# Optimization experiments

Hardware: AMD Instinct MI355X
Metric: run time of the kernel (lower is better)

The kernel has to match this reference:

```python
import jax, jax.numpy as jnp
import numpy as np

N = 20000        # num nodes
E = 320000       # num edges (avg degree 16)
INPUT_DIM = 256
D = 512          # d_model
FF = 2048        # dim_feedforward
OUT = 128        # output_linear out features
HDIM = 8         # LiteMLA per-head dim
KS = 5           # LiteMLA scale kernel size (scales=(5,))


def _layernorm(x, g, b, eps=1e-5):
    m = x.mean(-1, keepdims=True)
    v = ((x - m) ** 2).mean(-1, keepdims=True)
    return (x - m) * jax.lax.rsqrt(v + eps) * g + b


def _pos_encoding():
    # sin/cos table, d_model even branch of PositionalEncoding
    pos = np.arange(N, dtype=np.float32)[:, None]
    div = np.exp(np.arange(0, D, 2, dtype=np.float32) * (-np.log(10000.0) / D))
    pe = np.zeros((N, D), np.float32)
    pe[:, 0::2] = np.sin(pos * div)
    pe[:, 1::2] = np.cos(pos * div)
    return jnp.asarray(pe)


def _lite_mla(h, W_qkv, conv_w, W_proj, b_proj):
    # ReLU linear attention with one extra conv scale (kernel 5), per EfficientViT LiteMLA
    n, d = h.shape
    qkv = h @ W_qkv                               # [N, 3D]
    xc = qkv.T[None]                              # [1, 3D, N]
    ms = jax.lax.conv_general_dilated(
        xc, conv_w, window_strides=(1,), padding='SAME',
        feature_group_count=3 * D)                # depthwise conv over node axis
    ms = ms[0].T                                  # [N, 3D]
    full = jnp.concatenate([qkv, ms], axis=1)     # [N, 6D]
    heads = full.shape[1] // (3 * HDIM)           # 2 * D / HDIM
    t = full.reshape(n, heads, 3, HDIM)
    q = jax.nn.relu(t[:, :, 0])
    k = jax.nn.relu(t[:, :, 1])
    v = t[:, :, 2]
    v1 = jnp.concatenate([v, jnp.ones_like(v[..., :1])], axis=-1)  # append denom row
    kv = jnp.einsum('nhd,nhe->hde', k, v1)        # [h, HDIM, HDIM+1]
    o = jnp.einsum('nhd,hde->nhe', q, kv)         # [N, h, HDIM+1]
    o = o[..., :HDIM] / (o[..., HDIM:] + 1e-15)
    o = o.reshape(n, heads * HDIM)                # [N, 2D]
    return o @ W_proj + b_proj


def _fwd(x, edge_attr, pe, W_in, b_in, W_qkv, conv_w, W_proj, b_proj,
         g1, beta1, W1, bf1, W2, bf2, g2, beta2, W_out, b_out,
         edge_index, num_nodes):
    n = num_nodes
    h = x @ W_in + b_in
    h = h + pe[:n]                                # positional encoding (dropout=eval)
    # add self loops with weight 1
    loop = jnp.arange(n)
    row = jnp.concatenate([edge_index[0], loop])
    col = jnp.concatenate([edge_index[1], loop])
    w = jnp.concatenate([edge_attr, jnp.ones((n,), edge_attr.dtype)])
    # symmetric normalization: D^-1/2 W D^-1/2
    deg = jax.ops.segment_sum(w, row, num_segments=n)
    dis = jnp.where(deg > 0, jax.lax.rsqrt(jnp.maximum(deg, 1e-12)), 0.0)
    nw = dis[row] * w * dis[col]
    # attention + FFN (post-norm residuals as written)
    src2 = _lite_mla(h, W_qkv, conv_w, W_proj, b_proj)
    src = h + _layernorm(src2, g1, beta1)
    ff = jax.nn.relu(src @ W1 + bf1) @ W2 + bf2
    src = src + _layernorm(ff, g2, beta2)
    # sparse adjacency matmul: out[i] = sum_{e: row=i} nw_e * src[col_e]
    agg = jax.ops.segment_sum(nw[:, None] * src[col], row, num_segments=n)
    return jax.nn.relu(agg) @ W_out + b_out      # [N, OUT]


def setup_inputs() -> dict:
    key = jax.random.key(0)
    ks = jax.random.split(key, 10)
    s = lambda i, *sh: jax.random.normal(ks[i], sh, jnp.float32) * 0.02
    f32 = jnp.float32
    return {
        'x': jax.random.normal(ks[0], (N, INPUT_DIM), f32),
        'edge_index': jax.random.randint(ks[1], (2, E), 0, N),
        'edge_attr': jax.random.uniform(ks[2], (E,), f32),
        'num_nodes': N,
        'pe': _pos_encoding(),
        'W_in': s(3, INPUT_DIM, D), 'b_in': jnp.zeros((D,), f32),
        'W_qkv': s(4, D, 3 * D),
        'conv_w': s(5, 3 * D, 1, KS),
        'W_proj': s(6, 2 * D, D), 'b_proj': jnp.zeros((D,), f32),
        'g1': jnp.ones((D,), f32), 'beta1': jnp.zeros((D,), f32),
        'W1': s(7, D, FF), 'bf1': jnp.zeros((FF,), f32),
        'W2': s(8, FF, D), 'bf2': jnp.zeros((D,), f32),
        'g2': jnp.ones((D,), f32), 'beta2': jnp.zeros((D,), f32),
        'W_out': s(9, D, OUT), 'b_out': jnp.zeros((OUT,), f32),
    }


def reference(x, edge_index, edge_attr, num_nodes, pe, W_in, b_in, W_qkv, conv_w,
              W_proj, b_proj, g1, beta1, W1, bf1, W2, bf2, g2, beta2, W_out, b_out):
    return _fwd(x, edge_attr, pe, W_in, b_in, W_qkv, conv_w, W_proj, b_proj,
                g1, beta1, W1, bf1, W2, bf2, g2, beta2, W_out, b_out,
                edge_index, num_nodes)
```

## Files before the change

kernel.cpp:

```cpp
#include <hip/hip_runtime.h>

#define N_NODES 20000
#define N_EDGES 320000
#define DIN     256
#define DMODEL  512
#define TD      1536
#define FFD     2048
#define DOUT    128

typedef _Float16 f16;
typedef f16 f16x8 __attribute__((ext_vector_type(8)));
typedef f16 f16x4 __attribute__((ext_vector_type(4)));
typedef f16 f16x2 __attribute__((ext_vector_type(2)));
typedef float f32x4 __attribute__((ext_vector_type(4)));

__device__ __forceinline__ void cstore(float* p, float v) { *p = v; }
__device__ __forceinline__ void cstore(f16* p, float v)   { *p = (f16)v; }

#if defined(__has_builtin)
#if __has_builtin(__builtin_amdgcn_global_load_lds)
#define USE_GLOAD_LDS 1
#endif
#endif

template<typename TC, int HAS_BIAS, int HAS_ADD, int DO_RELU>
__global__ __launch_bounds__(256)
void gemm_mfma(const f16* __restrict__ A, const f16* __restrict__ Bt,
               const float* __restrict__ bias, const float* __restrict__ addmat,
               TC* __restrict__ C, int M, int N, int K)
{
    __shared__ f16 smem[32768];
    const int tid  = threadIdx.x;
    const int lane = tid & 63;
    const int wid  = tid >> 6;
    const int wm = wid >> 1, wn = wid & 1;

    const int nwg  = gridDim.x;
    const int bid  = blockIdx.x;
    const int q    = nwg >> 3, rres = nwg & 7;
    const int xcd  = bid & 7,  slot = bid >> 3;
    const int wgid = (xcd < rres ? xcd * (q + 1)
                                 : rres * (q + 1) + (xcd - rres) * q) + slot;
    const int ntn  = N >> 7;
    const int m0 = (wgid / ntn) * 128, n0 = (wgid % ntn) * 128;

    f32x4 acc[4][4];
    #pragma unroll
    for (int i = 0; i < 4; ++i)
        #pragma unroll
        for (int j = 0; j < 4; ++j)
            acc[i][j] = (f32x4)0.0f;

    const int r  = lane & 15;
    const int kg = lane >> 4;
    const int px = (kg ^ ((r >> 1) & 3)) << 3;

#ifdef USE_GLOAD_LDS
    const int seg0 = wid * 2, seg1 = wid * 2 + 1;
    const int row0 = seg0 * 16 + (lane >> 2);
    const int row1 = seg1 * 16 + (lane >> 2);
    const int kc0  = (lane & 3) ^ ((row0 >> 1) & 3);
    const int kc1  = (lane & 3) ^ ((row1 >> 1) & 3);
    const f16* a0 = A  + (size_t)(m0 + row0) * K + kc0 * 8;
    const f16* a1 = A  + (size_t)(m0 + row1) * K + kc1 * 8;
    const f16* b0 = Bt + (size_t)(n0 + row0) * K + kc0 * 8;
    const f16* b1 = Bt + (size_t)(n0 + row1) * K + kc1 * 8;

    auto stage = [&](int buf, int k0) {
        f16* as = smem + buf * 4096;
        f16* bs = smem + 16384 + buf * 4096;
        __builtin_amdgcn_global_load_lds(
            (const __attribute__((address_space(1))) void*)(a0 + k0),
            (__attribute__((address_space(3))) void*)&as[seg0 * 512], 16, 0, 0);
        __builtin_amdgcn_global_load_lds(
            (const __attribute__((address_space(1))) void*)(a1 + k0),
            (__attribute__((address_space(3))) void*)&as[seg1 * 512], 16, 0, 0);
        __builtin_amdgcn_global_load_lds(
            (const __attribute__((address_space(1))) void*)(b0 + k0),
            (__attribute__((address_space(3))) void*)&bs[seg0 * 512], 16, 0, 0);
        __builtin_amdgcn_global_load_lds(
            (const __attribute__((address_space(1))) void*)(b1 + k0),
            (__attribute__((address_space(3))) void*)&bs[seg1 * 512], 16, 0, 0);
    };

    const int NT = K >> 5;
    stage(0, 0);
    if (NT > 1) stage(1, 32);
    for (int kt = 0; kt < NT; ++kt) {
        const int cur = kt & 3;
        if (kt + 2 < NT) {
            stage((kt + 2) & 3, (kt + 2) << 5);
            asm volatile("s_waitcnt vmcnt(8)" ::: "memory");
        } else if (kt + 1 < NT) {
            asm volatile("s_waitcnt vmcnt(4)" ::: "memory");
        } else {
            asm volatile("s_waitcnt vmcnt(0)" ::: "memory");
        }
        __builtin_amdgcn_s_barrier();
        __builtin_amdgcn_sched_barrier(0);
        const f16* as = smem + cur * 4096;
        const f16* bs = smem + 16384 + cur * 4096;
        f16x8 af[4], bfr[4];
        #pragma unroll
        for (int m = 0; m < 4; ++m)
            af[m] = *(const f16x8*)(&as[(wm * 64 + m * 16 + r) * 32 + px]);
        #pragma unroll
        for (int n = 0; n < 4; ++n)
            bfr[n] = *(const f16x8*)(&bs[(wn * 64 + n * 16 + r) * 32 + px]);
        #pragma unroll
        for (int m = 0; m < 4; ++m)
            #pragma unroll
            for (int n = 0; n < 4; ++n)
                acc[m][n] = __builtin_amdgcn_mfma_f32_16x16x32_f16(
                    af[m], bfr[n], acc[m][n], 0, 0, 0);
    }
#else
    for (int k0 = 0; k0 < K; k0 += 32) {
        #pragma unroll
        for (int it = 0; it < 2; ++it) {
            const int c   = tid + it * 256;
            const int row = c >> 2, kc = c & 3;
            const int widx = row * 32 + ((kc ^ ((row >> 1) & 3)) << 3);
            f16x8 va = {0, 0, 0, 0, 0, 0, 0, 0};
            const int ga = m0 + row;
            if (ga < M) va = *(const f16x8*)(A + (size_t)ga * K + k0 + kc * 8);
            *(f16x8*)(&smem[widx]) = va;
            const f16x8 vb = *(const f16x8*)(Bt + (size_t)(n0 + row) * K + k0 + kc * 8);
            *(f16x8*)(&smem[16384 + widx]) = vb;
        }
        __syncthreads();
        f16x8 af[4], bfr[4];
        #pragma unroll
        for (int m = 0; m < 4; ++m)
            af[m] = *(const f16x8*)(&smem[(wm * 64 + m * 16 + r) * 32 + px]);
        #pragma unroll
        for (int n = 0; n < 4; ++n)
            bfr[n] = *(const f16x8*)(&smem[16384 + (wn * 64 + n * 16 + r) * 32 + px]);
        #pragma unroll
        for (int m = 0; m < 4; ++m)
            #pragma unroll
            for (int n = 0; n < 4; ++n)
                acc[m][n] = __builtin_amdgcn_mfma_f32_16x16x32_f16(
                    af[m], bfr[n], acc[m][n], 0, 0, 0);
        __syncthreads();
    }
#endif

    const int rq = lane >> 4;
    if constexpr (sizeof(TC) == 2) {
        __syncthreads();
        #pragma unroll
        for (int m = 0; m < 4; ++m) {
            #pragma unroll
            for (int rr = 0; rr < 4; ++rr) {
                const int rl = wm * 64 + m * 16 + rq * 4 + rr;
                #pragma unroll
                for (int n = 0; n < 4; ++n) {
                    const int cl = wn * 64 + n * 16 + (lane & 15);
                    float v = acc[m][n][rr];
                    if (HAS_BIAS) v += bias[n0 + cl];
                    if (HAS_ADD && (m0 + rl) < M) v += addmat[(size_t)(m0 + rl) * N + n0 + cl];
                    if (DO_RELU) v = fmaxf(v, 0.f);
                    smem[rl * 128 + cl] = (f16)v;
                }
            }
        }
        __syncthreads();
        #pragma unroll
        for (int i = 0; i < 8; ++i) {
            const int ch  = tid + i * 256;
            const int row = ch >> 4;
            const int cc  = (ch & 15) << 3;
            if (m0 + row < M)
                *(f16x8*)((f16*)C + (size_t)(m0 + row) * N + n0 + cc) =
                    *(const f16x8*)(&smem[row * 128 + cc]);
        }
    } else {
        #pragma unroll
        for (int m = 0; m < 4; ++m) {
            #pragma unroll
            for (int rr = 0; rr < 4; ++rr) {
                const int row = m0 + wm * 64 + m * 16 + rq * 4 + rr;
                if (row >= M) continue;
                #pragma unroll
                for (int n = 0; n < 4; ++n) {
                    const int col = n0 + wn * 64 + n * 16 + (lane & 15);
                    float v = acc[m][n][rr];
                    if (HAS_BIAS) v += bias[col];
                    if (HAS_ADD)  v += addmat[(size_t)row * N + col];
                    if (DO_RELU)  v = fmaxf(v, 0.f);
                    cstore(&C[(size_t)row * N + col], v);
                }
            }
        }
    }
}

__global__ void wt_kernel(const float* __restrict__ W, f16* __restrict__ Wt, int K, int N)
{
    __shared__ float t[32][33];
    const int k0 = blockIdx.x * 32, n0 = blockIdx.y * 32;
    const int tx = threadIdx.x & 31, ty = threadIdx.x >> 5;
    #pragma unroll
    for (int i = ty; i < 32; i += 8) {
        const int k = k0 + i;
        if (k < K && n0 + tx < N) t[i][tx] = W[(size_t)k * N + n0 + tx];
    }
    __syncthreads();
    #pragma unroll
    for (int i = ty; i < 32; i += 8) {
        const int n = n0 + i;
        if (n < N && k0 + tx < K) Wt[(size_t)n * K + k0 + tx] = (f16)t[tx][i];
    }
}

__global__ void f2h_kernel(const float* __restrict__ in, f16* __restrict__ out, int n)
{
    const int i = (blockIdx.x * 256 + threadIdx.x) * 4;
    if (i < n) {
        const float4 v = *(const float4*)(in + i);
        out[i + 0] = (f16)v.x; out[i + 1] = (f16)v.y;
        out[i + 2] = (f16)v.z; out[i + 3] = (f16)v.w;
    }
}

#define KV_CHUNK 32
#define KV_BLOCKS (N_NODES / KV_CHUNK)
__global__ __launch_bounds__(256, 2)
void kv_fused_kernel(const f16* __restrict__ qkv, const float* __restrict__ cw,
                     f16* __restrict__ q_all, float* __restrict__ kvg,
                     float* __restrict__ kv_part)
{
    __shared__ f16 rows[5][TD];
    const int tid = threadIdx.x;
    const int n0 = blockIdx.x * KV_CHUNK;
    const int h = tid >> 1, d0 = (tid & 1) * 4;

    float wk[4][5], wv[8][5], wq[8][5];
    if (h >= 64) {
        const int cb = (h - 64) * 24;
        #pragma unroll
        for (int dd = 0; dd < 4; ++dd)
            #pragma unroll
            for (int t = 0; t < 5; ++t)
                wk[dd][t] = cw[(cb + 8 + d0 + dd) * 5 + t];
        #pragma unroll
        for (int e = 0; e < 8; ++e)
            #pragma unroll
            for (int t = 0; t < 5; ++t)
                wv[e][t] = cw[(cb + 16 + e) * 5 + t];
    }
    if (tid >= 64 && tid < 128) {
        const int cb = (tid - 64) * 24;
        #pragma unroll
        for (int d = 0; d < 8; ++d)
            #pragma unroll
            for (int t = 0; t < 5; ++t)
                wq[d][t] = cw[(cb + d) * 5 + t];
    }

    for (int r = n0 - 2; r <= n0 + 2; ++r) {
        const int slot = ((r % 5) + 5) % 5;
        if (tid < 192) {
            f16x8 v = {0, 0, 0, 0, 0, 0, 0, 0};
            if (r >= 0 && r < N_NODES)
                v = *(const f16x8*)(qkv + (size_t)r * TD + tid * 8);
            *(f16x8*)(&rows[slot][tid * 8]) = v;
        }
    }
    __syncthreads();

    float acc[36] = {};

    for (int i = 0; i < KV_CHUNK; ++i) {
        const int n = n0 + i;

        f16x8 pre = {0, 0, 0, 0, 0, 0, 0, 0};
        const bool doPre = (i < KV_CHUNK - 1) && (tid < 192);
        if (doPre && (n + 3) < N_NODES)
            pre = *(const f16x8*)(qkv + (size_t)(n + 3) * TD + tid * 8);

        const f16* wr[5] = { rows[(((n - 2) % 5) + 5) % 5],
                             rows[(((n - 1) % 5) + 5) % 5],
                             rows[n % 5],
                             rows[(n + 1) % 5],
                             rows[(n + 2) % 5] };

        float kv4[4], vv[8];
        if (h < 64) {
            const int cb = h * 24;
            const f16x4 kd = *(const f16x4*)(wr[2] + cb + 8 + d0);
            const f16x8 vd = *(const f16x8*)(wr[2] + cb + 16);
            #pragma unroll
            for (int dd = 0; dd < 4; ++dd) kv4[dd] = fmaxf((float)kd[dd], 0.f);
            #pragma unroll
            for (int e = 0; e < 8; ++e) vv[e] = (float)vd[e];
        } else {
            const int cb = (h - 64) * 24;
            f16x4 ka[5]; f16x8 va[5];
            #pragma unroll
            for (int t = 0; t < 5; ++t) {
                ka[t] = *(const f16x4*)(wr[t] + cb + 8 + d0);
                va[t] = *(const f16x8*)(wr[t] + cb + 16);
            }
            #pragma unroll
            for (int dd = 0; dd < 4; ++dd) {
                float s = 0.f;
                #pragma unroll
                for (int t = 0; t < 5; ++t) s = fmaf(wk[dd][t], (float)ka[t][dd], s);
                kv4[dd] = fmaxf(s, 0.f);
            }
            #pragma unroll
            for (int e = 0; e < 8; ++e) {
                float s = 0.f;
                #pragma unroll
                for (int t = 0; t < 5; ++t) s = fmaf(wv[e][t], (float)va[t][e], s);
                vv[e] = s;
            }
        }
        #pragma unroll
        for (int dd = 0; dd < 4; ++dd) {
            #pragma unroll
            for (int e = 0; e < 8; ++e)
                acc[dd * 9 + e] = fmaf(kv4[dd], vv[e], acc[dd * 9 + e]);
            acc[dd * 9 + 8] += kv4[dd];
        }

        if (tid < 128) {
            f16x8 qv;
            if (tid < 64) {
                qv = *(const f16x8*)(wr[2] + tid * 24);
                #pragma unroll
                for (int d = 0; d < 8; ++d)
                    qv[d] = qv[d] > (f16)0 ? qv[d] : (f16)0;
            } else {
                const int cb = (tid - 64) * 24;
                f16x8 qa[5];
                #pragma unroll
                for (int t = 0; t < 5; ++t) qa[t] = *(const f16x8*)(wr[t] + cb);
                #pragma unroll
                for (int d = 0; d < 8; ++d) {
                    float s = 0.f;
                    #pragma unroll
                    for (int t = 0; t < 5; ++t) s = fmaf(wq[d][t], (float)qa[t][d], s);
                    qv[d] = (f16)fmaxf(s, 0.f);
                }
            }
            *(f16x8*)(q_all + (size_t)n * 1024 + tid * 8) = qv;
        }

        __syncthreads();
        if (doPre)
            *(f16x8*)(&rows[(n + 3) % 5][tid * 8]) = pre;
        __syncthreads();
    }

    if (kv_part) {
        float* dst = kv_part + (size_t)blockIdx.x * 9216 + tid * 36;
        #pragma unroll
        for (int i = 0; i < 36; ++i) dst[i] = acc[i];
    } else {
        #pragma unroll
        for (int dd = 0; dd < 4; ++dd)
            #pragma unroll
            for (int e = 0; e < 9; ++e)
                atomicAdd(&kvg[h * 72 + (d0 + dd) * 9 + e], acc[dd * 9 + e]);
    }
}

__global__ void kv_reduce_kernel(const float* __restrict__ kv_part,
                                 float* __restrict__ kvg)
{
    const int j = blockIdx.x * 256 + threadIdx.x;
    float s = 0.f;
    for (int b = 0; b < KV_BLOCKS; ++b)
        s += kv_part[(size_t)b * 9216 + j];
    kvg[j] = s;
}

__global__ __launch_bounds__(256)
void attn_o_kernel(const f16* __restrict__ q_all, const float* __restrict__ kvg,
                   f16* __restrict__ o)
{
    __shared__ float kvt[72][128];
    const int tid = threadIdx.x;
    for (int i = tid; i < 9216; i += 256) {
        const int hh = i & 127, j = i >> 7;
        kvt[j][hh] = kvg[hh * 72 + j];
    }
    __syncthreads();
    const int h = tid & 127, sub = tid >> 7;
    for (int nb = blockIdx.x; nb < N_NODES / 2; nb += gridDim.x) {
        const int n = nb * 2 + sub;
        const f16x8 qv8 = *(const f16x8*)(q_all + (size_t)n * 1024 + h * 8);
        float q[8];
        #pragma unroll
        for (int d = 0; d < 8; ++d) q[d] = (float)qv8[d];
        float num[8], den = 0.f;
        #pragma unroll
        for (int e = 0; e < 8; ++e) {
            float s = 0.f;
            #pragma unroll
            for (int d = 0; d < 8; ++d) s = fmaf(q[d], kvt[d * 9 + e][h], s);
            num[e] = s;
        }
        #pragma unroll
        for (int d = 0; d < 8; ++d) den = fmaf(q[d], kvt[d * 9 + 8][h], den);
        const float rinv = 1.f / (den + 1e-15f);
        f16x8 ov;
        #pragma unroll
        for (int e = 0; e < 8; ++e) ov[e] = (f16)(num[e] * rinv);
        *(f16x8*)(o + (size_t)n * 1024 + h * 8) = ov;
    }
}

__global__ void ln_res_kernel(const f16* __restrict__ y, const f16* __restrict__ resid,
                              const float* __restrict__ g, const float* __restrict__ b,
                              f16* __restrict__ out_h)
{
    const int row = blockIdx.x;
    const int tid = threadIdx.x;
    const f16* yr = y + (size_t)row * DMODEL;
    const float v0 = (float)yr[tid], v1 = (float)yr[tid + 256];
    __shared__ float red[4], red2[4];
    float s = v0 + v1;
    #pragma unroll
    for (int o = 32; o > 0; o >>= 1) s += __shfl_down(s, o);
    if ((tid & 63) == 0) red[tid >> 6] = s;
    __syncthreads();
    const float mean = (red[0] + red[1] + red[2] + red[3]) * (1.0f / DMODEL);
    const float d0 = v0 - mean, d1 = v1 - mean;
    float q = d0 * d0 + d1 * d1;
    #pragma unroll
    for (int o = 32; o > 0; o >>= 1) q += __shfl_down(q, o);
    if ((tid & 63) == 0) red2[tid >> 6] = q;
    __syncthreads();
    const float var = (red2[0] + red2[1] + red2[2] + red2[3]) * (1.0f / DMODEL);
    const float inv = rsqrtf(var + 1e-5f);
    const f16* rr = resid + (size_t)row * DMODEL;
    const float o0 = (float)rr[tid]       + d0 * inv * g[tid]       + b[tid];
    const float o1 = (float)rr[tid + 256] + d1 * inv * g[tid + 256] + b[tid + 256];
    f16* oh = out_h + (size_t)row * DMODEL;
    oh[tid] = (f16)o0;
    oh[tid + 256] = (f16)o1;
}

__global__ void deg_init_kernel(float* __restrict__ deg)
{
    const int i = blockIdx.x * 256 + threadIdx.x;
    if (i < N_NODES) deg[i] = 1.0f;
}

__global__ void deg_acc_kernel(const int* __restrict__ eirow, const float* __restrict__ ea,
                               float* __restrict__ deg)
{
    const int e = blockIdx.x * 256 + threadIdx.x;
    if (e < N_EDGES) atomicAdd(&deg[eirow[e]], ea[e]);
}

__global__ void dis_kernel(const float* __restrict__ deg, float* __restrict__ dis)
{
    const int i = blockIdx.x * 256 + threadIdx.x;
    if (i < N_NODES) dis[i] = rsqrtf(deg[i]);
}

__global__ void count_kernel(const int* __restrict__ eirow, int* __restrict__ cnt)
{
    const int e = blockIdx.x * 256 + threadIdx.x;
    if (e < N_EDGES) atomicAdd(&cnt[eirow[e]], 1);
}

__global__ void scan_kernel(const int* __restrict__ cnt, int* __restrict__ rowstart,
                            int* __restrict__ cursor)
{
    __shared__ int ls[1024];
    const int tid = threadIdx.x;
    const int base = tid * 20;
    int local[20];
    int s = 0;
    #pragma unroll
    for (int i = 0; i < 20; ++i) {
        const int idx = base + i;
        const int v = (idx < N_NODES) ? cnt[idx] : 0;
        local[i] = s;
        s += v;
    }
    ls[tid] = s;
    __syncthreads();
    for (int off = 1; off < 1024; off <<= 1) {
        const int v = (tid >= off) ? ls[tid - off] : 0;
        __syncthreads();
        ls[tid] += v;
        __syncthreads();
    }
    const int excl = (tid == 0) ? 0 : ls[tid - 1];
    #pragma unroll
    for (int i = 0; i < 20; ++i) {
        const int idx = base + i;
        if (idx < N_NODES) {
            const int st = excl + local[i];
            rowstart[idx] = st;
            cursor[idx] = st;
        }
    }
    if (tid == 1023) rowstart[N_NODES] = ls[1023];
}

__global__ void scatter_kernel(const int* __restrict__ eirow, int* __restrict__ cursor,
                               int* __restrict__ sorted)
{
    const int e = blockIdx.x * 256 + threadIdx.x;
    if (e < N_EDGES) {
        const int r = eirow[e];
        const int p = atomicAdd(&cursor[r], 1);
        sorted[p] = e;
    }
}

__global__ __launch_bounds__(256)
void agg_kernel(const f16* __restrict__ srcf_h, const int* __restrict__ eicol,
                const float* __restrict__ ea, const float* __restrict__ dis,
                const int* __restrict__ rowstart, const int* __restrict__ sorted,
                f16* __restrict__ agg)
{
    __shared__ int   cbuf[256];
    __shared__ float wbuf[256];
    __shared__ float part[4][512];
    const int i = blockIdx.x;
    const int tid = threadIdx.x;
    const int lane = tid & 63, wv = tid >> 6;
    const float di = dis[i];
    const int s = rowstart[i];
    const int deg = rowstart[i + 1] - s;

    float acc[8] = {};
    for (int base = 0; base < deg; base += 256) {
        const int m = min(256, deg - base);
        if (tid < m) {
            const int e = sorted[s + base + tid];
            const int c = eicol[e];
            cbuf[tid] = c;
            wbuf[tid] = di * ea[e] * dis[c];
        }
        __syncthreads();
        #pragma unroll 2
        for (int p = wv; p < m; p += 4) {
            const int c = cbuf[p];
            const float w = wbuf[p];
            const f16x8 v = *(const f16x8*)(srcf_h + (size_t)c * DMODEL + lane * 8);
            #pragma unroll
            for (int j = 0; j < 8; ++j) acc[j] = fmaf(w, (float)v[j], acc[j]);
        }
        __syncthreads();
    }
    #pragma unroll
    for (int j = 0; j < 8; ++j) part[wv][lane * 8 + j] = acc[j];
    __syncthreads();
    const float wself = di * di;
    const f16x2 vs = *(const f16x2*)(srcf_h + (size_t)i * DMODEL + tid * 2);
    float a0 = wself * (float)vs[0], a1 = wself * (float)vs[1];
    #pragma unroll
    for (int w = 0; w < 4; ++w) {
        a0 += part[w][tid * 2];
        a1 += part[w][tid * 2 + 1];
    }
    f16x2 o;
    o[0] = (f16)fmaxf(a0, 0.f);
    o[1] = (f16)fmaxf(a1, 0.f);
    *(f16x2*)(agg + (size_t)i * DMODEL + tid * 2) = o;
}

static constexpr size_t OFF_HH    = 0;
static constexpr size_t OFF_FF    = 20480000ull;
static constexpr size_t OFF_QKV   = 40960000ull;
static constexpr size_t OFF_SRC2  = 40960000ull;
static constexpr size_t OFF_FFH   = 61440000ull;
static constexpr size_t OFF_AGG   = 61440000ull;
static constexpr size_t OFF_XH    = 102400000ull;
static constexpr size_t OFF_ATTN  = 102400000ull;
static constexpr size_t WT_IN     = 143360000ull;
static constexpr size_t WT_QKV    = 143622144ull;
static constexpr size_t WT_PROJ   = 145195008ull;
static constexpr size_t WT_W1     = 146243584ull;
static constexpr size_t WT_W2     = 148340736ull;
static constexpr size_t WT_OUT    = 150437888ull;
static constexpr size_t OFF_KV    = 150568960ull;
static constexpr size_t OFF_DEG   = 150605824ull;
static constexpr size_t OFF_DIS   = 150685824ull;
static constexpr size_t OFF_RS    = 150765824ull;
static constexpr size_t OFF_CUR   = 150845888ull;
static constexpr size_t OFF_CNT   = 150925888ull;
static constexpr size_t OFF_SORT  = 151005888ull;
static constexpr size_t OFF_KVP   = 152285888ull;
static constexpr size_t WS_NEED_KVP = 175325888ull;

extern "C" void kernel_launch(void* const* d_in, const int* in_sizes, int n_in,
                              void* d_out, int out_size, void* d_ws, size_t ws_size,
                              hipStream_t stream)
{
    const float* x      = (const float*)d_in[0];
    const int*   ei     = (const int*)d_in[1];
    const float* ea     = (const float*)d_in[2];
    const float* pe     = (const float*)d_in[4];
    const float* W_in   = (const float*)d_in[5];
    const float* b_in   = (const float*)d_in[6];
    const float* W_qkv  = (const float*)d_in[7];
    const float* conv_w = (const float*)d_in[8];
    const float* W_proj = (const float*)d_in[9];
    const float* b_proj = (const float*)d_in[10];
    const float* g1     = (const float*)d_in[11];
    const float* beta1  = (const float*)d_in[12];
    const float* W1     = (const float*)d_in[13];
    const float* bf1    = (const float*)d_in[14];
    const float* W2     = (const float*)d_in[15];
    const float* bf2    = (const float*)d_in[16];
    const float* g2     = (const float*)d_in[17];
    const float* beta2  = (const float*)d_in[18];
    const float* W_out  = (const float*)d_in[19];
    const float* b_out  = (const float*)d_in[20];

    char* ws = (char*)d_ws;
    f16*   h_h    = (f16*)(ws + OFF_HH);
    f16*   ff     = (f16*)(ws + OFF_FF);
    f16*   qkv    = (f16*)(ws + OFF_QKV);
    f16*   src2   = (f16*)(ws + OFF_SRC2);
    f16*   ffh    = (f16*)(ws + OFF_FFH);
    f16*   agg    = (f16*)(ws + OFF_AGG);
    f16*   x_h    = (f16*)(ws + OFF_XH);
    f16*   q_all  = (f16*)(ws + OFF_ATTN);
    f16*   wt_in   = (f16*)(ws + WT_IN);
    f16*   wt_qkv  = (f16*)(ws + WT_QKV);
    f16*   wt_proj = (f16*)(ws + WT_PROJ);
    f16*   wt_w1   = (f16*)(ws + WT_W1);
    f16*   wt_w2   = (f16*)(ws + WT_W2);
    f16*   wt_out  = (f16*)(ws + WT_OUT);
    float* kvg    = (float*)(ws + OFF_KV);
    float* deg    = (float*)(ws + OFF_DEG);
    float* dis    = (float*)(ws + OFF_DIS);
    int*   rs     = (int*)(ws + OFF_RS);
    int*   cur    = (int*)(ws + OFF_CUR);
    int*   cnt    = (int*)(ws + OFF_CNT);
    int*   sorted = (int*)(ws + OFF_SORT);
    float* outp   = (float*)d_out;

    const bool twoStage = (ws_size >= WS_NEED_KVP);
    float* kv_part = twoStage ? (float*)(ws + OFF_KVP) : nullptr;

    const int* eirow = ei;
    const int* eicol = ei + N_EDGES;

    if (!twoStage)
        hipMemsetAsync(kvg, 0, 9216 * sizeof(float), stream);
    hipMemsetAsync(cnt, 0, N_NODES * sizeof(int), stream);

    wt_kernel<<<dim3(DIN / 32,   DMODEL / 32), 256, 0, stream>>>(W_in,   wt_in,   DIN,    DMODEL);
    wt_kernel<<<dim3(DMODEL / 32, TD / 32),    256, 0, stream>>>(W_qkv,  wt_qkv,  DMODEL, TD);
    wt_kernel<<<dim3(1024 / 32,  DMODEL / 32), 256, 0, stream>>>(W_proj, wt_proj, 1024,   DMODEL);
    wt_kernel<<<dim3(DMODEL / 32, FFD / 32),   256, 0, stream>>>(W1,     wt_w1,   DMODEL, FFD);
    wt_kernel<<<dim3(FFD / 32,   DMODEL / 32), 256, 0, stream>>>(W2,     wt_w2,   FFD,    DMODEL);
    wt_kernel<<<dim3(DMODEL / 32, DOUT / 32),  256, 0, stream>>>(W_out,  wt_out,  DMODEL, DOUT);
    f2h_kernel<<<(N_NODES * DIN) / 1024, 256, 0, stream>>>(x, x_h, N_NODES * DIN);

    const int MT = (N_NODES + 127) / 128;

    gemm_mfma<f16, 1, 1, 0><<<MT * (DMODEL / 128), 256, 0, stream>>>(
        x_h, wt_in, b_in, pe, h_h, N_NODES, DMODEL, DIN);
    gemm_mfma<f16, 0, 0, 0><<<MT * (TD / 128), 256, 0, stream>>>(
        h_h, wt_qkv, nullptr, nullptr, qkv, N_NODES, TD, DMODEL);
    kv_fused_kernel<<<KV_BLOCKS, 256, 0, stream>>>(qkv, conv_w, q_all, kvg, kv_part);
    if (twoStage)
        kv_reduce_kernel<<<36, 256, 0, stream>>>(kv_part, kvg);
    attn_o_kernel<<<2500, 256, 0, stream>>>(q_all, kvg, q_all);
    gemm_mfma<f16, 1, 0, 0><<<MT * (DMODEL / 128), 256, 0, stream>>>(
        q_all, wt_proj, b_proj, nullptr, src2, N_NODES, DMODEL, 1024);
    ln_res_kernel<<<N_NODES, 256, 0, stream>>>(src2, h_h, g1, beta1, src2);
    gemm_mfma<f16, 1, 0, 1><<<MT * (FFD / 128), 256, 0, stream>>>(
        src2, wt_w1, bf1, nullptr, ffh, N_NODES, FFD, DMODEL);
    gemm_mfma<f16, 1, 0, 0><<<MT * (DMODEL / 128), 256, 0, stream>>>(
        ffh, wt_w2, bf2, nullptr, ff, N_NODES, DMODEL, FFD);
    ln_res_kernel<<<N_NODES, 256, 0, stream>>>(ff, src2, g2, beta2, ff);
    deg_init_kernel<<<(N_NODES + 255) / 256, 256, 0, stream>>>(deg);
    deg_acc_kernel<<<(N_EDGES + 255) / 256, 256, 0, stream>>>(eirow, ea, deg);
    dis_kernel<<<(N_NODES + 255) / 256, 256, 0, stream>>>(deg, dis);
    count_kernel<<<(N_EDGES + 255) / 256, 256, 0, stream>>>(eirow, cnt);
    scan_kernel<<<1, 1024, 0, stream>>>(cnt, rs, cur);
    scatter_kernel<<<(N_EDGES + 255) / 256, 256, 0, stream>>>(eirow, cur, sorted);
    agg_kernel<<<N_NODES, 256, 0, stream>>>(ff, eicol, ea, dis, rs, sorted, agg);
    gemm_mfma<float, 1, 0, 0><<<MT * (DOUT / 128), 256, 0, stream>>>(
        agg, wt_out, b_out, nullptr, outp, N_NODES, DOUT, DMODEL);
}
```

Measured before the change: 627.1 us.

## Load GEMM B operand directly into registers with prefetch, bypassing LDS

The MFMA GEMM now stages only the A tile through LDS. Each wave reads its B fragments straight from global memory into registers, double-buffered one k-step ahead, and the vmcnt waits are adjusted for the new load counts. The aim is to halve LDS traffic and LDS allocation, which can allow higher occupancy, and to remove the LDS write/read round trip for B. In exchange, waves that share a B column slice each fetch it separately from global/L2, the per-lane 16-byte loads stride across rows, and register pressure goes up.

```diff
diff --git a/kernel.cpp b/kernel.cpp
--- a/kernel.cpp
+++ b/kernel.cpp
@@ -29,7 +29,7 @@
                const float* __restrict__ bias, const float* __restrict__ addmat,
                TC* __restrict__ C, int M, int N, int K)
 {
-    __shared__ f16 smem[32768];
+    __shared__ f16 smem[16384];
     const int tid  = threadIdx.x;
     const int lane = tid & 63;
     const int wid  = tid >> 6;
@@ -61,58 +61,58 @@
     const int row1 = seg1 * 16 + (lane >> 2);
     const int kc0  = (lane & 3) ^ ((row0 >> 1) & 3);
     const int kc1  = (lane & 3) ^ ((row1 >> 1) & 3);
-    const f16* a0 = A  + (size_t)(m0 + row0) * K + kc0 * 8;
-    const f16* a1 = A  + (size_t)(m0 + row1) * K + kc1 * 8;
-    const f16* b0 = Bt + (size_t)(n0 + row0) * K + kc0 * 8;
-    const f16* b1 = Bt + (size_t)(n0 + row1) * K + kc1 * 8;
-
-    auto stage = [&](int buf, int k0) {
+    const f16* a0 = A + (size_t)(m0 + row0) * K + kc0 * 8;
+    const f16* a1 = A + (size_t)(m0 + row1) * K + kc1 * 8;
+    const f16* bq = Bt + (size_t)(n0 + wn * 64 + r) * K + kg * 8;
+
+    auto stageA = [&](int buf, int k0) {
         f16* as = smem + buf * 4096;
-        f16* bs = smem + 16384 + buf * 4096;
         __builtin_amdgcn_global_load_lds(
             (const __attribute__((address_space(1))) void*)(a0 + k0),
             (__attribute__((address_space(3))) void*)&as[seg0 * 512], 16, 0, 0);
         __builtin_amdgcn_global_load_lds(
             (const __attribute__((address_space(1))) void*)(a1 + k0),
             (__attribute__((address_space(3))) void*)&as[seg1 * 512], 16, 0, 0);
-        __builtin_amdgcn_global_load_lds(
-            (const __attribute__((address_space(1))) void*)(b0 + k0),
-            (__attribute__((address_space(3))) void*)&bs[seg0 * 512], 16, 0, 0);
-        __builtin_amdgcn_global_load_lds(
-            (const __attribute__((address_space(1))) void*)(b1 + k0),
-            (__attribute__((address_space(3))) void*)&bs[seg1 * 512], 16, 0, 0);
     };
 
     const int NT = K >> 5;
-    stage(0, 0);
-    if (NT > 1) stage(1, 32);
+    f16x8 bcur[4], bnext[4];
+    stageA(0, 0);
+    #pragma unroll
+    for (int n = 0; n < 4; ++n)
+        bcur[n] = *(const f16x8*)(bq + (size_t)n * 16 * K);
+    stageA(1, 32);
     for (int kt = 0; kt < NT; ++kt) {
-        const int cur = kt & 3;
+        if (kt + 1 < NT) {
+            #pragma unroll
+            for (int n = 0; n < 4; ++n)
+                bnext[n] = *(const f16x8*)(bq + (size_t)n * 16 * K + (kt + 1) * 32);
+        }
         if (kt + 2 < NT) {
-            stage((kt + 2) & 3, (kt + 2) << 5);
+            stageA((kt + 2) & 3, (kt + 2) << 5);
             asm volatile("s_waitcnt vmcnt(8)" ::: "memory");
         } else if (kt + 1 < NT) {
-            asm volatile("s_waitcnt vmcnt(4)" ::: "memory");
+            asm volatile("s_waitcnt vmcnt(6)" ::: "memory");
         } else {
             asm volatile("s_waitcnt vmcnt(0)" ::: "memory");
         }
         __builtin_amdgcn_s_barrier();
         __builtin_amdgcn_sched_barrier(0);
-        const f16* as = smem + cur * 4096;
-        const f16* bs = smem + 16384 + cur * 4096;
-        f16x8 af[4], bfr[4];
+        const f16* as = smem + (kt & 3) * 4096;
+        f16x8 af[4];
         #pragma unroll
         for (int m = 0; m < 4; ++m)
             af[m] = *(const f16x8*)(&as[(wm * 64 + m * 16 + r) * 32 + px]);
         #pragma unroll
-        for (int n = 0; n < 4; ++n)
-            bfr[n] = *(const f16x8*)(&bs[(wn * 64 + n * 16 + r) * 32 + px]);
-        #pragma unroll
         for (int m = 0; m < 4; ++m)
             #pragma unroll
             for (int n = 0; n < 4; ++n)
                 acc[m][n] = __builtin_amdgcn_mfma_f32_16x16x32_f16(
-                    af[m], bfr[n], acc[m][n], 0, 0, 0);
+                    af[m], bcur[n], acc[m][n], 0, 0, 0);
+        if (kt + 1 < NT) {
+            #pragma unroll
+            for (int n = 0; n < 4; ++n) bcur[n] = bnext[n];
+        }
     }
 #else
     for (int k0 = 0; k0 < K; k0 += 32) {
@@ -125,8 +125,6 @@
             const int ga = m0 + row;
             if (ga < M) va = *(const f16x8*)(A + (size_t)ga * K + k0 + kc * 8);
             *(f16x8*)(&smem[widx]) = va;
-            const f16x8 vb = *(const f16x8*)(Bt + (size_t)(n0 + row) * K + k0 + kc * 8);
-            *(f16x8*)(&smem[16384 + widx]) = vb;
         }
         __syncthreads();
         f16x8 af[4], bfr[4];
@@ -135,7 +133,7 @@
             af[m] = *(const f16x8*)(&smem[(wm * 64 + m * 16 + r) * 32 + px]);
         #pragma unroll
         for (int n = 0; n < 4; ++n)
-            bfr[n] = *(const f16x8*)(&smem[16384 + (wn * 64 + n * 16 + r) * 32 + px]);
+            bfr[n] = *(const f16x8*)(Bt + (size_t)(n0 + wn * 64 + n * 16 + r) * K + k0 + kg * 8);
         #pragma unroll
         for (int m = 0; m < 4; ++m)
             #pragma unroll
```

Result: slower. 749.3 us (+19.5%).
